# Performance work log

Measured on AMD Instinct MI355X. Metric: run time of the kernel, lower is better.

The kernel has to match this reference:

```python
import jax, jax.numpy as jnp
import numpy as np

NEG_INF = -1e30  # stand-in for -inf that is safe under fp16/bf16 softmax


def setup_inputs() -> dict:
    key = jax.random.key(0)
    k1, k2, k3, k4, k5 = jax.random.split(key, 5)
    B, Tq, Tk, DIN, DOUT = 8, 1024, 4096, 1024, 256
    dec = jax.random.normal(k1, (B, Tq, DIN), dtype=jnp.float32)
    emb = jax.random.normal(k2, (B, Tk, DOUT), dtype=jnp.float32)
    emask = jax.random.randint(k3, (B, Tk), 0, 2, dtype=jnp.int32)
    W = jax.random.normal(k4, (DOUT, DIN), dtype=jnp.float32) * (1.0 / np.sqrt(DIN))
    b = jax.random.normal(k5, (DOUT,), dtype=jnp.float32) * 0.01
    return {"dec": dec, "emb": emb, "emask": emask, "W": W, "b": b}


def reference(dec, emb, emask, W, b):
    # Linear projection: [B,Tq,DIN] @ [DIN,DOUT] + b -> [B,Tq,DOUT]
    decsmall = jnp.einsum('bqi,oi->bqo', dec, W) + b
    # Scores: [B,Tq,Tk]
    unnorm = jnp.einsum('bqo,bko->bqk', decsmall, emb)
    # mask: positions where emask == 0 are disallowed
    masked = jnp.where((emask == 0)[:, None, :], NEG_INF, unnorm)
    attn = jax.nn.softmax(masked, axis=2)
    out = jnp.einsum('bqk,bko->bqo', attn, emb)
    return (out, attn)
```

## Files before the change

### kernel.cpp

```cpp
#include <hip/hip_runtime.h>
#include <hip/hip_bf16.h>
#include <hip/hip_fp16.h>

typedef unsigned short u16;
typedef __attribute__((ext_vector_type(8))) short short8;
typedef __attribute__((ext_vector_type(8))) u16 u16x8;
typedef __attribute__((ext_vector_type(4))) u16 u16x4;
typedef __attribute__((ext_vector_type(8))) _Float16 half8;
typedef __attribute__((ext_vector_type(4))) float f32x4;

#define NB 8
#define TQn 1024
#define TKn 4096
#define DINn 1024
#define DOUTn 256
#define NROWS (NB * TQn)
#define NKB (TKn / 128)
#define EXPSHIFT 40.0f

#define DEV static __device__ __forceinline__

DEV u16 f2bf(float x) {
    __hip_bfloat16 h = __float2bfloat16(x);
    return *reinterpret_cast<u16*>(&h);
}
DEV float bf2f(u16 u) {
    __hip_bfloat16 h;
    *reinterpret_cast<u16*>(&h) = u;
    return __bfloat162float(h);
}
DEV void split2(float x, u16& hi, u16& lo) {
    u16 h = f2bf(x);
    float hf = bf2f(h);
    hi = h;
    lo = f2bf(x - hf);
}
DEV void split4(const float4 v, u16x4& h, u16x4& l) {
    u16 h0, l0, h1, l1, h2, l2, h3, l3;
    split2(v.x, h0, l0);
    split2(v.y, h1, l1);
    split2(v.z, h2, l2);
    split2(v.w, h3, l3);
    h = (u16x4){h0, h1, h2, h3};
    l = (u16x4){l0, l1, l2, l3};
}

__global__ __launch_bounds__(256) void k_embT(const float* __restrict__ emb,
                                              _Float16* __restrict__ embT) {
    __shared__ float tile[64][65];
    const int b = blockIdx.z;
    const int k0 = blockIdx.x * 64;
    const int o0 = blockIdx.y * 64;
    const int t = threadIdx.x;
    const int c = t & 63;
    const int r0 = t >> 6;
#pragma unroll
    for (int i = 0; i < 16; i++) {
        int r = r0 + i * 4;
        tile[c][r] = emb[((size_t)b * TKn + k0 + r) * DOUTn + o0 + c];
    }
    __syncthreads();
#pragma unroll
    for (int i = 0; i < 16; i++) {
        int r = r0 + i * 4;
        embT[((size_t)b * DOUTn + o0 + r) * TKn + k0 + c] = (_Float16)tile[r][c];
    }
}

__global__ __launch_bounds__(256) void k_linear(const float* __restrict__ dec,
                                                const float* __restrict__ W,
                                                const float* __restrict__ bias,
                                                u16* __restrict__ ds_hi,
                                                u16* __restrict__ ds_lo) {
    __shared__ u16 sAh[128][40], sAl[128][40], sBh[64][40], sBl[64][40];
    const int t = threadIdx.x;
    const int m0 = blockIdx.x * 128;
    const int n0 = blockIdx.y * 64;
    const int w = t >> 6, lane = t & 63;
    const int wr = w >> 1, wc = w & 1;
    const int lr = lane & 15, kg8 = (lane >> 4) * 8;

    f32x4 acc[4][2];
#pragma unroll
    for (int m = 0; m < 4; m++)
#pragma unroll
        for (int n = 0; n < 2; n++) acc[m][n] = (f32x4){0.f, 0.f, 0.f, 0.f};

    for (int k0 = 0; k0 < DINn; k0 += 32) {
        __syncthreads();
#pragma unroll
        for (int i = 0; i < 4; i++) {
            int f = i * 256 + t;
            int row = f >> 3, c4 = (f & 7) * 4;
            const float4 v = *reinterpret_cast<const float4*>(
                dec + (size_t)(m0 + row) * DINn + k0 + c4);
            u16x4 h, l;
            split4(v, h, l);
            *reinterpret_cast<u16x4*>(&sAh[row][c4]) = h;
            *reinterpret_cast<u16x4*>(&sAl[row][c4]) = l;
        }
#pragma unroll
        for (int i = 0; i < 2; i++) {
            int f = i * 256 + t;
            int row = f >> 3, c4 = (f & 7) * 4;
            const float4 v = *reinterpret_cast<const float4*>(
                W + (size_t)(n0 + row) * DINn + k0 + c4);
            u16x4 h, l;
            split4(v, h, l);
            *reinterpret_cast<u16x4*>(&sBh[row][c4]) = h;
            *reinterpret_cast<u16x4*>(&sBl[row][c4]) = l;
        }
        __syncthreads();
        short8 ah[4], al[4], bh[2], bl[2];
#pragma unroll
        for (int m = 0; m < 4; m++) {
            int row = wr * 64 + m * 16 + lr;
            ah[m] = *reinterpret_cast<const short8*>(&sAh[row][kg8]);
            al[m] = *reinterpret_cast<const short8*>(&sAl[row][kg8]);
        }
#pragma unroll
        for (int n = 0; n < 2; n++) {
            int row = wc * 32 + n * 16 + lr;
            bh[n] = *reinterpret_cast<const short8*>(&sBh[row][kg8]);
            bl[n] = *reinterpret_cast<const short8*>(&sBl[row][kg8]);
        }
#pragma unroll
        for (int m = 0; m < 4; m++)
#pragma unroll
            for (int n = 0; n < 2; n++) {
                acc[m][n] = __builtin_amdgcn_mfma_f32_16x16x32_bf16(ah[m], bh[n], acc[m][n], 0, 0, 0);
                acc[m][n] = __builtin_amdgcn_mfma_f32_16x16x32_bf16(ah[m], bl[n], acc[m][n], 0, 0, 0);
                acc[m][n] = __builtin_amdgcn_mfma_f32_16x16x32_bf16(al[m], bh[n], acc[m][n], 0, 0, 0);
            }
    }
#pragma unroll
    for (int m = 0; m < 4; m++) {
#pragma unroll
        for (int n = 0; n < 2; n++) {
            int colg = n0 + wc * 32 + n * 16 + lr;
            float bv = bias[colg];
#pragma unroll
            for (int r = 0; r < 4; r++) {
                int rowg = m0 + wr * 64 + m * 16 + (lane >> 4) * 4 + r;
                float v = acc[m][n][r] + bv;
                u16 h, l;
                split2(v, h, l);
                ds_hi[(size_t)rowg * DOUTn + colg] = h;
                ds_lo[(size_t)rowg * DOUTn + colg] = l;
            }
        }
    }
}

__global__ __launch_bounds__(256) void k_scores_exp(const u16* __restrict__ ds_hi,
                                                    const u16* __restrict__ ds_lo,
                                                    const float* __restrict__ emb,
                                                    const int* __restrict__ emask,
                                                    float* __restrict__ attn,
                                                    float* __restrict__ partsum) {
    __shared__ u16 sAh[128][40], sAl[128][40], sBh[128][40], sBl[128][40];
    __shared__ float sSum[2][128];
    const int t = threadIdx.x;
    const int q0 = blockIdx.x * 128;
    const int kb = blockIdx.y;
    const int kb0 = kb * 128;
    const int b = blockIdx.z;
    const int w = t >> 6, lane = t & 63;
    const int wr = w >> 1, wc = w & 1;
    const int lr = lane & 15, g = lane >> 4, kg8 = g * 8;

    f32x4 acc[4][4];
#pragma unroll
    for (int m = 0; m < 4; m++)
#pragma unroll
        for (int n = 0; n < 4; n++) acc[m][n] = (f32x4){0.f, 0.f, 0.f, 0.f};

    for (int o0 = 0; o0 < DOUTn; o0 += 32) {
        __syncthreads();
#pragma unroll
        for (int i = 0; i < 2; i++) {
            int f8 = i * 256 + t;
            int row = f8 >> 2, c8 = (f8 & 3) * 8;
            size_t src = (size_t)(b * TQn + q0 + row) * DOUTn + o0 + c8;
            *reinterpret_cast<u16x8*>(&sAh[row][c8]) =
                *reinterpret_cast<const u16x8*>(ds_hi + src);
            *reinterpret_cast<u16x8*>(&sAl[row][c8]) =
                *reinterpret_cast<const u16x8*>(ds_lo + src);
        }
#pragma unroll
        for (int i = 0; i < 4; i++) {
            int f = i * 256 + t;
            int row = f >> 3, c4 = (f & 7) * 4;
            const float4 v = *reinterpret_cast<const float4*>(
                emb + (size_t)(b * TKn + kb0 + row) * DOUTn + o0 + c4);
            u16x4 h, l;
            split4(v, h, l);
            *reinterpret_cast<u16x4*>(&sBh[row][c4]) = h;
            *reinterpret_cast<u16x4*>(&sBl[row][c4]) = l;
        }
        __syncthreads();
        short8 ah[4], al[4], bh[4], bl[4];
#pragma unroll
        for (int m = 0; m < 4; m++) {
            int row = wr * 64 + m * 16 + lr;
            ah[m] = *reinterpret_cast<const short8*>(&sAh[row][kg8]);
            al[m] = *reinterpret_cast<const short8*>(&sAl[row][kg8]);
        }
#pragma unroll
        for (int n = 0; n < 4; n++) {
            int row = wc * 64 + n * 16 + lr;
            bh[n] = *reinterpret_cast<const short8*>(&sBh[row][kg8]);
            bl[n] = *reinterpret_cast<const short8*>(&sBl[row][kg8]);
        }
#pragma unroll
        for (int m = 0; m < 4; m++)
#pragma unroll
            for (int n = 0; n < 4; n++) {
                acc[m][n] = __builtin_amdgcn_mfma_f32_16x16x32_bf16(ah[m], bh[n], acc[m][n], 0, 0, 0);
                acc[m][n] = __builtin_amdgcn_mfma_f32_16x16x32_bf16(ah[m], bl[n], acc[m][n], 0, 0, 0);
                acc[m][n] = __builtin_amdgcn_mfma_f32_16x16x32_bf16(al[m], bh[n], acc[m][n], 0, 0, 0);
            }
    }
    const int* em = emask + (size_t)b * TKn;
    float* pout = attn + ((size_t)(b * TQn + q0)) * TKn + kb0;
    float rowAcc[4][4];
#pragma unroll
    for (int m = 0; m < 4; m++)
#pragma unroll
        for (int r = 0; r < 4; r++) rowAcc[m][r] = 0.f;

#pragma unroll
    for (int n = 0; n < 4; n++) {
        int colL = wc * 64 + n * 16 + lr;
        int mk = em[kb0 + colL];
#pragma unroll
        for (int m = 0; m < 4; m++) {
#pragma unroll
            for (int r = 0; r < 4; r++) {
                int rowL = wr * 64 + m * 16 + g * 4 + r;
                float p = mk ? __expf(acc[m][n][r] - EXPSHIFT) : 0.f;
                pout[(size_t)rowL * TKn + colL] = p;
                rowAcc[m][r] += p;
            }
        }
    }
#pragma unroll
    for (int m = 0; m < 4; m++) {
#pragma unroll
        for (int r = 0; r < 4; r++) {
            float v = rowAcc[m][r];
            v += __shfl_xor(v, 1);
            v += __shfl_xor(v, 2);
            v += __shfl_xor(v, 4);
            v += __shfl_xor(v, 8);
            if (lr == 0) sSum[wc][wr * 64 + m * 16 + g * 4 + r] = v;
        }
    }
    __syncthreads();
    if (t < 128) {
        partsum[(size_t)kb * NROWS + (size_t)b * TQn + q0 + t] =
            sSum[0][t] + sSum[1][t];
    }
}

__global__ __launch_bounds__(256) void k_rowsum(const float* __restrict__ partsum,
                                                float* __restrict__ inv_sum) {
    int row = blockIdx.x * 256 + threadIdx.x;
    float s = 0.f;
#pragma unroll
    for (int kb = 0; kb < NKB; kb++) s += partsum[(size_t)kb * NROWS + row];
    inv_sum[row] = 1.0f / s;
}

__global__ __launch_bounds__(256) void k_pv2(float* __restrict__ attn,
                                             const _Float16* __restrict__ embT,
                                             const float* __restrict__ inv_sum,
                                             float* __restrict__ partial) {
    __shared__ u16 sA[64][40];
    __shared__ u16 sB[256][40];
    const int t = threadIdx.x;
    const int w = t >> 6, lane = t & 63;
    const int lr = lane & 15, g = lane >> 4, kg8 = g * 8;
    const int q0 = blockIdx.x * 64;
    const int kc = blockIdx.y;
    const int b = blockIdx.z;
    const int kbase = kc * 1024;

    f32x4 acc[4][4];
#pragma unroll
    for (int m = 0; m < 4; m++)
#pragma unroll
        for (int n = 0; n < 4; n++) acc[m][n] = (f32x4){0.f, 0.f, 0.f, 0.f};

    for (int ks = 0; ks < 1024; ks += 32) {
        __syncthreads();
#pragma unroll
        for (int i = 0; i < 2; i++) {
            int f = i * 256 + t;
            int row = f >> 3, c4 = (f & 7) * 4;
            size_t gaddr = ((size_t)(b * TQn + q0 + row)) * TKn + kbase + ks + c4;
            f32x4 v = *reinterpret_cast<const f32x4*>(attn + gaddr);
            float inv = inv_sum[(size_t)b * TQn + q0 + row];
            v = v * inv;
            *reinterpret_cast<f32x4*>(attn + gaddr) = v;
            u16x4 hv;
            hv[0] = __builtin_bit_cast(u16, (_Float16)v[0]);
            hv[1] = __builtin_bit_cast(u16, (_Float16)v[1]);
            hv[2] = __builtin_bit_cast(u16, (_Float16)v[2]);
            hv[3] = __builtin_bit_cast(u16, (_Float16)v[3]);
            *reinterpret_cast<u16x4*>(&sA[row][c4]) = hv;
        }
#pragma unroll
        for (int i = 0; i < 4; i++) {
            int f = i * 256 + t;
            int row = f >> 2, c8 = (f & 3) * 8;
            *reinterpret_cast<u16x8*>(&sB[row][c8]) = *reinterpret_cast<const u16x8*>(
                embT + ((size_t)(b * DOUTn + row)) * TKn + kbase + ks + c8);
        }
        __syncthreads();
        half8 a[4], bb[4];
#pragma unroll
        for (int m = 0; m < 4; m++)
            a[m] = *reinterpret_cast<const half8*>(&sA[m * 16 + lr][kg8]);
#pragma unroll
        for (int n = 0; n < 4; n++)
            bb[n] = *reinterpret_cast<const half8*>(&sB[w * 64 + n * 16 + lr][kg8]);
#pragma unroll
        for (int m = 0; m < 4; m++)
#pragma unroll
            for (int n = 0; n < 4; n++)
                acc[m][n] = __builtin_amdgcn_mfma_f32_16x16x32_f16(a[m], bb[n], acc[m][n], 0, 0, 0);
    }
#pragma unroll
    for (int m = 0; m < 4; m++) {
#pragma unroll
        for (int n = 0; n < 4; n++) {
            int col = w * 64 + n * 16 + lr;
#pragma unroll
            for (int r = 0; r < 4; r++) {
                size_t grow = (size_t)b * TQn + q0 + m * 16 + g * 4 + r;
                partial[((size_t)kc * NROWS + grow) * DOUTn + col] = acc[m][n][r];
            }
        }
    }
}

__global__ __launch_bounds__(256) void k_reduce(const float* __restrict__ partial,
                                                float* __restrict__ out) {
    const size_t stride = (size_t)NROWS * DOUTn;
    size_t i = ((size_t)blockIdx.x * 256 + threadIdx.x) * 4;
    f32x4 a0 = *reinterpret_cast<const f32x4*>(partial + i);
    f32x4 a1 = *reinterpret_cast<const f32x4*>(partial + stride + i);
    f32x4 a2 = *reinterpret_cast<const f32x4*>(partial + 2 * stride + i);
    f32x4 a3 = *reinterpret_cast<const f32x4*>(partial + 3 * stride + i);
    f32x4 s = (a0 + a1) + (a2 + a3);
    *reinterpret_cast<f32x4*>(out + i) = s;
}

extern "C" void kernel_launch(void* const* d_in, const int* in_sizes, int n_in,
                              void* d_out, int out_size, void* d_ws, size_t ws_size,
                              hipStream_t stream) {
    const float* dec = (const float*)d_in[0];
    const float* emb = (const float*)d_in[1];
    const int* emask = (const int*)d_in[2];
    const float* W = (const float*)d_in[3];
    const float* bias = (const float*)d_in[4];

    float* out = (float*)d_out;
    float* attn = out + (size_t)NROWS * DOUTn;

    char* wsb = (char*)d_ws;
    u16* ds_hi = (u16*)wsb;
    wsb += (size_t)NROWS * DOUTn * 2;
    u16* ds_lo = (u16*)wsb;
    wsb += (size_t)NROWS * DOUTn * 2;
    _Float16* embT = (_Float16*)wsb;
    wsb += (size_t)NB * DOUTn * TKn * 2;
    float* inv_sum = (float*)wsb;
    wsb += (size_t)NROWS * 4;
    float* partial = (float*)wsb;
    float* partsum = partial;

    k_embT<<<dim3(TKn / 64, DOUTn / 64, NB), 256, 0, stream>>>(emb, embT);
    k_linear<<<dim3(NROWS / 128, DOUTn / 64), 256, 0, stream>>>(dec, W, bias, ds_hi, ds_lo);
    k_scores_exp<<<dim3(TQn / 128, NKB, NB), 256, 0, stream>>>(ds_hi, ds_lo, emb, emask, attn, partsum);
    k_rowsum<<<dim3(NROWS / 256), 256, 0, stream>>>(partsum, inv_sum);
    k_pv2<<<dim3(TQn / 64, 4, NB), 256, 0, stream>>>(attn, embT, inv_sum, partial);
    k_reduce<<<dim3((NROWS * DOUTn / 4) / 256), 256, 0, stream>>>(partial, out);
}
```

Measured before the change: 209.8 us.

## Replace split-K PV with full-K 32-row tiles, drop reduce, pad LDS

The PV kernel now covers the full key length per block, using 32-query tiles and 512 threads, and writes the output directly. This removes the partial buffer and the separate reduce kernel. The change also narrows LDS row padding to 36 with 64-bit split loads and stores, remaps block indices so batch is the fastest-varying index (for L2 locality), and uses nontemporal stores for the attention writes. The trade-off is less MFMA work per wave, and each block now streams the whole embT slice for its batch.

```diff
diff --git a/kernel.cpp b/kernel.cpp
--- a/kernel.cpp
+++ b/kernel.cpp
@@ -4,10 +4,14 @@
 
 typedef unsigned short u16;
 typedef __attribute__((ext_vector_type(8))) short short8;
+typedef __attribute__((ext_vector_type(4))) short s16x4;
 typedef __attribute__((ext_vector_type(8))) u16 u16x8;
 typedef __attribute__((ext_vector_type(4))) u16 u16x4;
+typedef __attribute__((ext_vector_type(2))) u16 u16x2;
 typedef __attribute__((ext_vector_type(8))) _Float16 half8;
+typedef __attribute__((ext_vector_type(4))) _Float16 half4;
 typedef __attribute__((ext_vector_type(4))) float f32x4;
+typedef __attribute__((ext_vector_type(2))) float f32x2;
 
 #define NB 8
 #define TQn 1024
@@ -17,6 +21,7 @@
 #define NROWS (NB * TQn)
 #define NKB (TKn / 128)
 #define EXPSHIFT 40.0f
+#define LP 36
 
 #define DEV static __device__ __forceinline__
 
@@ -43,6 +48,26 @@
     split2(v.w, h3, l3);
     h = (u16x4){h0, h1, h2, h3};
     l = (u16x4){l0, l1, l2, l3};
+}
+DEV short8 ld8s(const u16* p) {
+    s16x4 a = *reinterpret_cast<const s16x4*>(p);
+    s16x4 b = *reinterpret_cast<const s16x4*>(p + 4);
+    short8 r;
+    r[0] = a[0]; r[1] = a[1]; r[2] = a[2]; r[3] = a[3];
+    r[4] = b[0]; r[5] = b[1]; r[6] = b[2]; r[7] = b[3];
+    return r;
+}
+DEV half8 ld8h(const u16* p) {
+    half4 a = *reinterpret_cast<const half4*>(p);
+    half4 b = *reinterpret_cast<const half4*>(p + 4);
+    half8 r;
+    r[0] = a[0]; r[1] = a[1]; r[2] = a[2]; r[3] = a[3];
+    r[4] = b[0]; r[5] = b[1]; r[6] = b[2]; r[7] = b[3];
+    return r;
+}
+DEV void st8(u16* p, u16x8 v) {
+    *reinterpret_cast<u16x4*>(p) = (u16x4){v[0], v[1], v[2], v[3]};
+    *reinterpret_cast<u16x4*>(p + 4) = (u16x4){v[4], v[5], v[6], v[7]};
 }
 
 __global__ __launch_bounds__(256) void k_embT(const float* __restrict__ emb,
@@ -72,13 +97,13 @@
                                                 const float* __restrict__ bias,
                                                 u16* __restrict__ ds_hi,
                                                 u16* __restrict__ ds_lo) {
-    __shared__ u16 sAh[128][40], sAl[128][40], sBh[64][40], sBl[64][40];
+    __shared__ u16 sAh[128][LP], sAl[128][LP], sBh[64][LP], sBl[64][LP];
     const int t = threadIdx.x;
     const int m0 = blockIdx.x * 128;
     const int n0 = blockIdx.y * 64;
     const int w = t >> 6, lane = t & 63;
     const int wr = w >> 1, wc = w & 1;
-    const int lr = lane & 15, kg8 = (lane >> 4) * 8;
+    const int lr = lane & 15, g = lane >> 4, kg8 = g * 8;
 
     f32x4 acc[4][2];
 #pragma unroll
@@ -115,14 +140,14 @@
 #pragma unroll
         for (int m = 0; m < 4; m++) {
             int row = wr * 64 + m * 16 + lr;
-            ah[m] = *reinterpret_cast<const short8*>(&sAh[row][kg8]);
-            al[m] = *reinterpret_cast<const short8*>(&sAl[row][kg8]);
+            ah[m] = ld8s(&sAh[row][kg8]);
+            al[m] = ld8s(&sAl[row][kg8]);
         }
 #pragma unroll
         for (int n = 0; n < 2; n++) {
             int row = wc * 32 + n * 16 + lr;
-            bh[n] = *reinterpret_cast<const short8*>(&sBh[row][kg8]);
-            bl[n] = *reinterpret_cast<const short8*>(&sBl[row][kg8]);
+            bh[n] = ld8s(&sBh[row][kg8]);
+            bl[n] = ld8s(&sBl[row][kg8]);
         }
 #pragma unroll
         for (int m = 0; m < 4; m++)
@@ -141,7 +166,7 @@
             float bv = bias[colg];
 #pragma unroll
             for (int r = 0; r < 4; r++) {
-                int rowg = m0 + wr * 64 + m * 16 + (lane >> 4) * 4 + r;
+                int rowg = m0 + wr * 64 + m * 16 + g * 4 + r;
                 float v = acc[m][n][r] + bv;
                 u16 h, l;
                 split2(v, h, l);
@@ -158,13 +183,15 @@
                                                     const int* __restrict__ emask,
                                                     float* __restrict__ attn,
                                                     float* __restrict__ partsum) {
-    __shared__ u16 sAh[128][40], sAl[128][40], sBh[128][40], sBl[128][40];
+    __shared__ u16 sAh[128][LP], sAl[128][LP], sBh[128][LP], sBl[128][LP];
     __shared__ float sSum[2][128];
     const int t = threadIdx.x;
-    const int q0 = blockIdx.x * 128;
-    const int kb = blockIdx.y;
+    const int flat = blockIdx.x + 8 * (blockIdx.y + 32 * blockIdx.z);
+    const int b = flat & 7;
+    const int rest = flat >> 3;
+    const int kb = rest & 31;
+    const int q0 = (rest >> 5) * 128;
     const int kb0 = kb * 128;
-    const int b = blockIdx.z;
     const int w = t >> 6, lane = t & 63;
     const int wr = w >> 1, wc = w & 1;
     const int lr = lane & 15, g = lane >> 4, kg8 = g * 8;
@@ -182,10 +209,8 @@
             int f8 = i * 256 + t;
             int row = f8 >> 2, c8 = (f8 & 3) * 8;
             size_t src = (size_t)(b * TQn + q0 + row) * DOUTn + o0 + c8;
-            *reinterpret_cast<u16x8*>(&sAh[row][c8]) =
-                *reinterpret_cast<const u16x8*>(ds_hi + src);
-            *reinterpret_cast<u16x8*>(&sAl[row][c8]) =
-                *reinterpret_cast<const u16x8*>(ds_lo + src);
+            st8(&sAh[row][c8], *reinterpret_cast<const u16x8*>(ds_hi + src));
+            st8(&sAl[row][c8], *reinterpret_cast<const u16x8*>(ds_lo + src));
         }
 #pragma unroll
         for (int i = 0; i < 4; i++) {
@@ -203,14 +228,14 @@
 #pragma unroll
         for (int m = 0; m < 4; m++) {
             int row = wr * 64 + m * 16 + lr;
-            ah[m] = *reinterpret_cast<const short8*>(&sAh[row][kg8]);
-            al[m] = *reinterpret_cast<const short8*>(&sAl[row][kg8]);
+            ah[m] = ld8s(&sAh[row][kg8]);
+            al[m] = ld8s(&sAl[row][kg8]);
         }
 #pragma unroll
         for (int n = 0; n < 4; n++) {
             int row = wc * 64 + n * 16 + lr;
-            bh[n] = *reinterpret_cast<const short8*>(&sBh[row][kg8]);
-            bl[n] = *reinterpret_cast<const short8*>(&sBl[row][kg8]);
+            bh[n] = ld8s(&sBh[row][kg8]);
+            bl[n] = ld8s(&sBl[row][kg8]);
         }
 #pragma unroll
         for (int m = 0; m < 4; m++)
@@ -239,7 +264,7 @@
             for (int r = 0; r < 4; r++) {
                 int rowL = wr * 64 + m * 16 + g * 4 + r;
                 float p = mk ? __expf(acc[m][n][r] - EXPSHIFT) : 0.f;
-                pout[(size_t)rowL * TKn + colL] = p;
+                __builtin_nontemporal_store(p, &pout[(size_t)rowL * TKn + colL]);
                 rowAcc[m][r] += p;
             }
         }
@@ -272,89 +297,65 @@
     inv_sum[row] = 1.0f / s;
 }
 
-__global__ __launch_bounds__(256) void k_pv2(float* __restrict__ attn,
+__global__ __launch_bounds__(512) void k_pv3(float* __restrict__ attn,
                                              const _Float16* __restrict__ embT,
                                              const float* __restrict__ inv_sum,
-                                             float* __restrict__ partial) {
-    __shared__ u16 sA[64][40];
-    __shared__ u16 sB[256][40];
+                                             float* __restrict__ out) {
+    __shared__ u16 sA[32][LP];
+    __shared__ u16 sB[256][LP];
     const int t = threadIdx.x;
+    const int flat = blockIdx.x + 32 * blockIdx.y;
+    const int b = flat & 7;
+    const int q0 = (flat >> 3) * 32;
     const int w = t >> 6, lane = t & 63;
     const int lr = lane & 15, g = lane >> 4, kg8 = g * 8;
-    const int q0 = blockIdx.x * 64;
-    const int kc = blockIdx.y;
-    const int b = blockIdx.z;
-    const int kbase = kc * 1024;
-
-    f32x4 acc[4][4];
-#pragma unroll
-    for (int m = 0; m < 4; m++)
-#pragma unroll
-        for (int n = 0; n < 4; n++) acc[m][n] = (f32x4){0.f, 0.f, 0.f, 0.f};
-
-    for (int ks = 0; ks < 1024; ks += 32) {
-        __syncthreads();
-#pragma unroll
-        for (int i = 0; i < 2; i++) {
-            int f = i * 256 + t;
-            int row = f >> 3, c4 = (f & 7) * 4;
-            size_t gaddr = ((size_t)(b * TQn + q0 + row)) * TKn + kbase + ks + c4;
-            f32x4 v = *reinterpret_cast<const f32x4*>(attn + gaddr);
-            float inv = inv_sum[(size_t)b * TQn + q0 + row];
+    const int rh = w >> 2;
+    const int oq = w & 3;
+    const u16* ebt = reinterpret_cast<const u16*>(embT);
+
+    const int arow = t >> 4, c2 = (t & 15) * 2;
+    const float inv = inv_sum[(size_t)b * TQn + q0 + arow];
+    float* pA = attn + ((size_t)(b * TQn + q0 + arow)) * TKn + c2;
+
+    f32x4 acc[4];
+#pragma unroll
+    for (int n = 0; n < 4; n++) acc[n] = (f32x4){0.f, 0.f, 0.f, 0.f};
+
+    for (int ks = 0; ks < TKn; ks += 32) {
+        __syncthreads();
+        {
+            f32x2 v = *reinterpret_cast<const f32x2*>(pA + ks);
             v = v * inv;
-            *reinterpret_cast<f32x4*>(attn + gaddr) = v;
-            u16x4 hv;
+            __builtin_nontemporal_store(v, reinterpret_cast<f32x2*>(pA + ks));
+            u16x2 hv;
             hv[0] = __builtin_bit_cast(u16, (_Float16)v[0]);
             hv[1] = __builtin_bit_cast(u16, (_Float16)v[1]);
-            hv[2] = __builtin_bit_cast(u16, (_Float16)v[2]);
-            hv[3] = __builtin_bit_cast(u16, (_Float16)v[3]);
-            *reinterpret_cast<u16x4*>(&sA[row][c4]) = hv;
-        }
-#pragma unroll
-        for (int i = 0; i < 4; i++) {
-            int f = i * 256 + t;
-            int row = f >> 2, c8 = (f & 3) * 8;
-            *reinterpret_cast<u16x8*>(&sB[row][c8]) = *reinterpret_cast<const u16x8*>(
-                embT + ((size_t)(b * DOUTn + row)) * TKn + kbase + ks + c8);
-        }
-        __syncthreads();
-        half8 a[4], bb[4];
-#pragma unroll
-        for (int m = 0; m < 4; m++)
-            a[m] = *reinterpret_cast<const half8*>(&sA[m * 16 + lr][kg8]);
-#pragma unroll
-        for (int n = 0; n < 4; n++)
-            bb[n] = *reinterpret_cast<const half8*>(&sB[w * 64 + n * 16 + lr][kg8]);
-#pragma unroll
-        for (int m = 0; m < 4; m++)
-#pragma unroll
-            for (int n = 0; n < 4; n++)
-                acc[m][n] = __builtin_amdgcn_mfma_f32_16x16x32_f16(a[m], bb[n], acc[m][n], 0, 0, 0);
-    }
-#pragma unroll
-    for (int m = 0; m < 4; m++) {
+            *reinterpret_cast<u16x2*>(&sA[arow][c2]) = hv;
+        }
+#pragma unroll
+        for (int i = 0; i < 2; i++) {
+            int f = i * 512 + t;
+            int brow = f >> 2, bc8 = (f & 3) * 8;
+            st8(&sB[brow][bc8], *reinterpret_cast<const u16x8*>(
+                                    ebt + (size_t)(b * DOUTn + brow) * TKn + ks + bc8));
+        }
+        __syncthreads();
+        half8 af = ld8h(&sA[rh * 16 + lr][kg8]);
 #pragma unroll
         for (int n = 0; n < 4; n++) {
-            int col = w * 64 + n * 16 + lr;
-#pragma unroll
-            for (int r = 0; r < 4; r++) {
-                size_t grow = (size_t)b * TQn + q0 + m * 16 + g * 4 + r;
-                partial[((size_t)kc * NROWS + grow) * DOUTn + col] = acc[m][n][r];
-            }
-        }
-    }
-}
-
-__global__ __launch_bounds__(256) void k_reduce(const float* __restrict__ partial,
-                                                float* __restrict__ out) {
-    const size_t stride = (size_t)NROWS * DOUTn;
-    size_t i = ((size_t)blockIdx.x * 256 + threadIdx.x) * 4;
-    f32x4 a0 = *reinterpret_cast<const f32x4*>(partial + i);
-    f32x4 a1 = *reinterpret_cast<const f32x4*>(partial + stride + i);
-    f32x4 a2 = *reinterpret_cast<const f32x4*>(partial + 2 * stride + i);
-    f32x4 a3 = *reinterpret_cast<const f32x4*>(partial + 3 * stride + i);
-    f32x4 s = (a0 + a1) + (a2 + a3);
-    *reinterpret_cast<f32x4*>(out + i) = s;
+            half8 bf = ld8h(&sB[oq * 64 + n * 16 + lr][kg8]);
+            acc[n] = __builtin_amdgcn_mfma_f32_16x16x32_f16(af, bf, acc[n], 0, 0, 0);
+        }
+    }
+#pragma unroll
+    for (int n = 0; n < 4; n++) {
+        int col = oq * 64 + n * 16 + lr;
+#pragma unroll
+        for (int r = 0; r < 4; r++) {
+            int rowL = rh * 16 + g * 4 + r;
+            out[((size_t)(b * TQn + q0 + rowL)) * DOUTn + col] = acc[n][r];
+        }
+    }
 }
 
 extern "C" void kernel_launch(void* const* d_in, const int* in_sizes, int n_in,
@@ -378,13 +379,11 @@
     wsb += (size_t)NB * DOUTn * TKn * 2;
     float* inv_sum = (float*)wsb;
     wsb += (size_t)NROWS * 4;
-    float* partial = (float*)wsb;
-    float* partsum = partial;
+    float* partsum = (float*)wsb;
 
     k_embT<<<dim3(TKn / 64, DOUTn / 64, NB), 256, 0, stream>>>(emb, embT);
     k_linear<<<dim3(NROWS / 128, DOUTn / 64), 256, 0, stream>>>(dec, W, bias, ds_hi, ds_lo);
     k_scores_exp<<<dim3(TQn / 128, NKB, NB), 256, 0, stream>>>(ds_hi, ds_lo, emb, emask, attn, partsum);
     k_rowsum<<<dim3(NROWS / 256), 256, 0, stream>>>(partsum, inv_sum);
-    k_pv2<<<dim3(TQn / 64, 4, NB), 256, 0, stream>>>(attn, embT, inv_sum, partial);
-    k_reduce<<<dim3((NROWS * DOUTn / 4) / 256), 256, 0, stream>>>(partial, out);
-}
+    k_pv3<<<dim3(TQn / 32, NB), 512, 0, stream>>>(attn, embT, inv_sum, out);
+}
```

After: 277.0 us. 1.32x slower.
